# Performance work log

Hardware: AMD Instinct MI355X
Metric: run time of the kernel (lower is better)

Reference implementation:

```python
import jax, jax.numpy as jnp
import numpy as np

EPS = 1e-5  # BatchNorm eps
TOPK = 256  # SoftThresholdingOperation topk


def conv1x1(x, W, b):
    # x: [B,C,H,W], W: [O,C], b: [O]
    return jnp.einsum('bchw,oc->bohw', x, W) + b[None, :, None, None]


def bn_relu(x, gamma, beta, mean, var):
    # inference-mode BatchNorm2d followed by ReLU
    inv = gamma / jnp.sqrt(var + EPS)
    return jax.nn.relu(x * inv[None, :, None, None] + (beta - mean * inv)[None, :, None, None])


def topk_sparsemax(x, k):
    # HSPA SoftThresholdingOperation: sparsemax restricted to top-k entries of last axis.
    k = min(k, x.shape[-1])
    vals = jax.lax.top_k(x, k)[0]                       # sorted descending, [..., k]
    cssv = jnp.cumsum(vals, axis=-1) - 1.0              # cumulative sum minus 1
    r = jnp.arange(1, k + 1, dtype=x.dtype)
    support = vals * r > cssv                           # support indicator
    k_sup = jnp.sum(support, axis=-1, keepdims=True)    # support size, int
    tau = jnp.take_along_axis(cssv, k_sup - 1, axis=-1) / k_sup.astype(x.dtype)
    return jnp.clip(x - tau, 0.0)                       # sparse attention weights


def setup_inputs() -> dict:
    key = jax.random.key(0)
    ks = jax.random.split(key, 10)
    B, C = 128, 256
    s = 1.0 / np.sqrt(C)
    return {
        'zf': jax.random.normal(ks[0], (B, C, 13, 13), jnp.float32),
        'xf': jax.random.normal(ks[1], (B, C, 25, 25), jnp.float32),
        'Wq': jax.random.normal(ks[2], (C, C), jnp.float32) * s,
        'bq': jnp.zeros((C,), jnp.float32),
        'Ws': jax.random.normal(ks[3], (C, C), jnp.float32) * s,
        'bs': jnp.zeros((C,), jnp.float32),
        'Wg': jax.random.normal(ks[4], (C, C), jnp.float32) * s,
        'bg': jnp.zeros((C,), jnp.float32),
        'g_gamma': jnp.ones((C,), jnp.float32),
        'g_beta': jnp.zeros((C,), jnp.float32),
        'g_mean': jnp.zeros((C,), jnp.float32),
        'g_var': jnp.ones((C,), jnp.float32),
        'Wf': jax.random.normal(ks[5], (C, 2 * C), jnp.float32) * (1.0 / np.sqrt(2 * C)),
        'bf': jnp.zeros((C,), jnp.float32),
        'f_gamma': jnp.ones((C,), jnp.float32),
        'f_beta': jnp.zeros((C,), jnp.float32),
        'f_mean': jnp.zeros((C,), jnp.float32),
        'f_var': jnp.ones((C,), jnp.float32),
    }


def reference(zf, xf, Wq, bq, Ws, bs, Wg, bg, g_gamma, g_beta, g_mean, g_var,
              Wf, bf, f_gamma, f_beta, f_mean, f_var):
    B, C, Hx, Wx = xf.shape
    _, _, Hz, Wz = zf.shape
    xf_trans = conv1x1(xf, Wq, bq)                      # query
    zf_trans = conv1x1(zf, Ws, bs)                      # support
    xf_g = bn_relu(conv1x1(xf, Wg, bg), g_gamma, g_beta, g_mean, g_var)
    zf_g = bn_relu(conv1x1(zf, Wg, bg), g_gamma, g_beta, g_mean, g_var)

    Nx, Nz = Hx * Wx, Hz * Wz
    zf_trans_p = zf_trans.reshape(B, C, Nz)             # [B,C,Nz]
    zf_g_p = zf_g.reshape(B, C, Nz)                     # [B,C,Nz]
    xf_trans_p = xf_trans.reshape(B, C, Nx)             # [B,C,Nx]

    similar = jnp.einsum('bcn,bcm->bnm', xf_trans_p, zf_trans_p)  # [B,Nx,Nz]
    score = topk_sparsemax(similar, TOPK)                          # sparse attn
    embedding = jnp.einsum('bnm,bcm->bcn', score, zf_g_p)          # [B,C,Nx]
    embedding = embedding.reshape(B, C, Hx, Wx)

    cat = jnp.concatenate([embedding, xf_g], axis=1)    # [B,2C,Hx,Wx]
    out = bn_relu(conv1x1(cat, Wf, bf), f_gamma, f_beta, f_mean, f_var)
    return out
```

## Files before the change

kernel.cpp:

```cpp
#include <hip/hip_runtime.h>
#include <math.h>

#define EPS 1e-5f

constexpr int Bb  = 128;
constexpr int C   = 256;
constexpr int Nz  = 169;
constexpr int Nx  = 625;
constexpr int NzP = 192;

typedef __bf16 bf16x8 __attribute__((ext_vector_type(8)));
typedef float  f32x4  __attribute__((ext_vector_type(4)));

__device__ __forceinline__ unsigned short f2bf(float f) {
    union { float f; unsigned u; } x; x.f = f;
    unsigned r = x.u + 0x7FFFu + ((x.u >> 16) & 1u);
    return (unsigned short)(r >> 16);
}
__device__ __forceinline__ float bf2f(unsigned short h) {
    union { unsigned u; float f; } x; x.u = ((unsigned)h) << 16;
    return x.f;
}

__global__ __launch_bounds__(256)
void prep_all(const float* __restrict__ zf,
              const float* __restrict__ Wq, const float* __restrict__ bq,
              const float* __restrict__ Ws, const float* __restrict__ bs,
              const float* __restrict__ Wg, const float* __restrict__ Wf,
              unsigned short* __restrict__ Wg_bf, unsigned short* __restrict__ Wf_bf,
              float* __restrict__ wv, float* __restrict__ wu, float* __restrict__ c0,
              unsigned short* __restrict__ Mhi, unsigned short* __restrict__ Mlo,
              float* __restrict__ U,
              unsigned short* __restrict__ zfT_hi, unsigned short* __restrict__ zfT_lo)
{
    __shared__ float T[64][65];
    const int bx = blockIdx.x, tid = threadIdx.x;

    if (bx < 512) {
        int i = bx * 256 + tid;
        if (i < C * C) Wg_bf[i] = f2bf(Wg[i]);
        if (i < C * 2 * C) Wf_bf[i] = f2bf(Wf[i]);
        return;
    }
    if (bx == 512) {
        float a = 0.f, b = 0.f;
        for (int o = 0; o < C; ++o) {
            a += Wq[o * C + tid] * bs[o];
            b += Ws[o * C + tid] * bq[o];
        }
        wv[tid] = a;
        wu[tid] = b;
        if (tid == 0) {
            float c = 0.f;
            for (int o = 0; o < C; ++o) c += bq[o] * bs[o];
            c0[0] = c;
        }
        return;
    }
    if (bx < 529) {
        const int t  = bx - 513;
        const int j0 = (t & 3) * 64, i0 = (t >> 2) * 64;
        const int tx = tid & 15, ty = tid >> 4;
        float (*Qs)[65] = (float(*)[65])&T[0][0];
        float (*Ss)[65] = (float(*)[65])&T[16][0];
        float acc[4][4] = {};

        for (int kc = 0; kc < C; kc += 16) {
            #pragma unroll
            for (int i = 0; i < 4; ++i) {
                int e = tid + 256 * i;
                int k = e >> 6, col = e & 63;
                Qs[k][col] = Wq[(size_t)(kc + k) * C + i0 + col];
                Ss[k][col] = Ws[(size_t)(kc + k) * C + j0 + col];
            }
            __syncthreads();
            #pragma unroll
            for (int k = 0; k < 16; ++k) {
                float a[4], bv[4];
                #pragma unroll
                for (int i = 0; i < 4; ++i) a[i] = Qs[k][ty * 4 + i];
                #pragma unroll
                for (int j = 0; j < 4; ++j) bv[j] = Ss[k][tx * 4 + j];
                #pragma unroll
                for (int i = 0; i < 4; ++i)
                    #pragma unroll
                    for (int j = 0; j < 4; ++j)
                        acc[i][j] = fmaf(a[i], bv[j], acc[i][j]);
            }
            __syncthreads();
        }
        #pragma unroll
        for (int i = 0; i < 4; ++i)
            #pragma unroll
            for (int j = 0; j < 4; ++j) {
                float v = acc[i][j];
                unsigned short h = f2bf(v);
                size_t idx = (size_t)(i0 + ty * 4 + i) * C + j0 + tx * 4 + j;
                Mhi[idx] = h;
                Mlo[idx] = f2bf(v - bf2f(h));
            }
        return;
    }
    if (bx < 657) {
        const int b = bx - 529, m = tid;
        if (m >= NzP) return;
        float s = 0.f;
        if (m < Nz) {
            const float* zb = zf + (size_t)b * C * Nz + m;
            float s0 = 0.f, s1 = 0.f, s2 = 0.f, s3 = 0.f;
            for (int c = 0; c < C; c += 4) {
                s0 += wu[c]     * zb[(size_t)c * Nz];
                s1 += wu[c + 1] * zb[(size_t)(c + 1) * Nz];
                s2 += wu[c + 2] * zb[(size_t)(c + 2) * Nz];
                s3 += wu[c + 3] * zb[(size_t)(c + 3) * Nz];
            }
            s = (s0 + s1) + (s2 + s3) + c0[0];
        }
        U[(size_t)b * NzP + m] = s;
        return;
    }
    {
        const int t  = bx - 657;
        const int n0 = (t % 3) * 64;
        const int c0v = ((t / 3) & 3) * 64;
        const int b  = t / 12;
        const float* Xb = zf + ((size_t)b * C + c0v) * Nz;
        #pragma unroll
        for (int i = 0; i < 16; ++i) {
            int e = tid + 256 * i;
            int c = e >> 6, n = e & 63;
            T[c][n] = (n0 + n < Nz) ? Xb[(size_t)c * Nz + n0 + n] : 0.f;
        }
        __syncthreads();
        #pragma unroll
        for (int i = 0; i < 16; ++i) {
            int e = tid + 256 * i;
            int n = e >> 6, c = e & 63;
            if (n0 + n < Nz) {
                float v = T[c][n];
                unsigned short h = f2bf(v);
                size_t idx = ((size_t)b * Nz + n0 + n) * C + c0v + c;
                zfT_hi[idx] = h;
                zfT_lo[idx] = f2bf(v - bf2f(h));
            }
        }
    }
}

__global__ __launch_bounds__(256)
void z_gemm(const unsigned short* __restrict__ Mhi,
            const unsigned short* __restrict__ Mlo,
            const unsigned short* __restrict__ Wg,
            const unsigned short* __restrict__ Bhi,
            const unsigned short* __restrict__ Blo,
            const float* __restrict__ wv,
            const float* __restrict__ bg, const float* __restrict__ g_gamma,
            const float* __restrict__ g_beta, const float* __restrict__ g_mean,
            const float* __restrict__ g_var,
            unsigned short* __restrict__ Yqh, unsigned short* __restrict__ Yql,
            unsigned short* __restrict__ Yg)
{
    __shared__ unsigned short Ah[64][40], Al[64][40], Ag[64][40];
    __shared__ unsigned short Bh[64][40], Bl[64][40];

    const int b   = blockIdx.z;
    const int n0  = blockIdx.x * 64;
    const int o0  = blockIdx.y * 64;
    const int tid = threadIdx.x;
    const int lane = tid & 63, wid = tid >> 6;
    const int wr = wid >> 1, wc = wid & 1;

    const unsigned short* Bhb = Bhi + (size_t)b * Nz * C;
    const unsigned short* Blb = Blo + (size_t)b * Nz * C;

    f32x4 accq[2][2], accg[2][2];
    #pragma unroll
    for (int i = 0; i < 2; ++i)
        #pragma unroll
        for (int j = 0; j < 2; ++j)
            #pragma unroll
            for (int e = 0; e < 4; ++e) { accq[i][j][e] = 0.f; accg[i][j][e] = 0.f; }

    const int srow = tid >> 2, sseg = tid & 3;
    const int lr = lane & 15, lk = (lane >> 4) * 8;

    for (int kc = 0; kc < C; kc += 32) {
        const int gk = kc + sseg * 8;
        *(int4*)&Ah[srow][sseg * 8] = *(const int4*)&Mhi[(size_t)(o0 + srow) * C + gk];
        *(int4*)&Al[srow][sseg * 8] = *(const int4*)&Mlo[(size_t)(o0 + srow) * C + gk];
        *(int4*)&Ag[srow][sseg * 8] = *(const int4*)&Wg[(size_t)(o0 + srow) * C + gk];

        const int gn = n0 + srow;
        int4 bv = make_int4(0, 0, 0, 0), blv = make_int4(0, 0, 0, 0);
        if (gn < Nz) {
            bv  = *(const int4*)&Bhb[(size_t)gn * C + gk];
            blv = *(const int4*)&Blb[(size_t)gn * C + gk];
        }
        *(int4*)&Bh[srow][sseg * 8] = bv;
        *(int4*)&Bl[srow][sseg * 8] = blv;
        __syncthreads();

        bf16x8 ah[2], al[2], ag[2], bh[2], bl[2];
        #pragma unroll
        for (int i = 0; i < 2; ++i) {
            ah[i] = *(const bf16x8*)&Ah[wr * 32 + i * 16 + lr][lk];
            al[i] = *(const bf16x8*)&Al[wr * 32 + i * 16 + lr][lk];
            ag[i] = *(const bf16x8*)&Ag[wr * 32 + i * 16 + lr][lk];
            bh[i] = *(const bf16x8*)&Bh[wc * 32 + i * 16 + lr][lk];
            bl[i] = *(const bf16x8*)&Bl[wc * 32 + i * 16 + lr][lk];
        }
        #pragma unroll
        for (int i = 0; i < 2; ++i)
            #pragma unroll
            for (int j = 0; j < 2; ++j) {
                accq[i][j] = __builtin_amdgcn_mfma_f32_16x16x32_bf16(al[i], bh[j], accq[i][j], 0, 0, 0);
                accq[i][j] = __builtin_amdgcn_mfma_f32_16x16x32_bf16(ah[i], bl[j], accq[i][j], 0, 0, 0);
                accq[i][j] = __builtin_amdgcn_mfma_f32_16x16x32_bf16(ah[i], bh[j], accq[i][j], 0, 0, 0);
                accg[i][j] = __builtin_amdgcn_mfma_f32_16x16x32_bf16(ag[i], bh[j], accg[i][j], 0, 0, 0);
            }
        __syncthreads();
    }

    const int lg = lane >> 4;
    #pragma unroll
    for (int i = 0; i < 2; ++i) {
        const int ob = o0 + wr * 32 + i * 16 + lg * 4;
        float bi[4], inv[4], sh[4], bgi[4];
        #pragma unroll
        for (int r = 0; r < 4; ++r) {
            int o = ob + r;
            bi[r] = wv[o];
            float iv = g_gamma[o] * rsqrtf(g_var[o] + EPS);
            inv[r] = iv; sh[r] = g_beta[o] - g_mean[o] * iv; bgi[r] = bg[o];
        }
        #pragma unroll
        for (int j = 0; j < 2; ++j) {
            const int gn = n0 + wc * 32 + j * 16 + lr;
            uint2 ph = make_uint2(0, 0), pl = make_uint2(0, 0), pg = make_uint2(0, 0);
            if (gn < Nz) {
                unsigned short h[4], l[4], g[4];
                #pragma unroll
                for (int r = 0; r < 4; ++r) {
                    float v = accq[i][j][r] + bi[r];
                    h[r] = f2bf(v);
                    l[r] = f2bf(v - bf2f(h[r]));
                    g[r] = f2bf(fmaxf(fmaf(accg[i][j][r] + bgi[r], inv[r], sh[r]), 0.f));
                }
                ph.x = (unsigned)h[0] | ((unsigned)h[1] << 16);
                ph.y = (unsigned)h[2] | ((unsigned)h[3] << 16);
                pl.x = (unsigned)l[0] | ((unsigned)l[1] << 16);
                pl.y = (unsigned)l[2] | ((unsigned)l[3] << 16);
                pg.x = (unsigned)g[0] | ((unsigned)g[1] << 16);
                pg.y = (unsigned)g[2] | ((unsigned)g[3] << 16);
            }
            size_t idx = ((size_t)b * NzP + gn) * C + ob;
            *(uint2*)&Yqh[idx] = ph;
            *(uint2*)&Yql[idx] = pl;
            *(uint2*)&Yg[idx]  = pg;
        }
    }
}

__global__ __launch_bounds__(256)
void zg2_gemm(const unsigned short* __restrict__ A, int aLd,
              const unsigned short* __restrict__ B1,
              unsigned short* __restrict__ Y, int N, int Nout, int K, int O)
{
    __shared__ unsigned short As[64][40];
    __shared__ unsigned short Bs[64][40];

    const int b   = blockIdx.z;
    const int n0  = blockIdx.x * 64;
    const int o0  = blockIdx.y * 64;
    const int tid = threadIdx.x;
    const int lane = tid & 63, wid = tid >> 6;
    const int wr = wid >> 1, wc = wid & 1;

    const unsigned short* B1b = B1 + (size_t)b * N * K;

    f32x4 acc[2][2];
    #pragma unroll
    for (int i = 0; i < 2; ++i)
        #pragma unroll
        for (int j = 0; j < 2; ++j)
            #pragma unroll
            for (int e = 0; e < 4; ++e) acc[i][j][e] = 0.f;

    const int srow = tid >> 2, sseg = tid & 3;
    const int lr = lane & 15, lk = (lane >> 4) * 8;

    for (int kc = 0; kc < K; kc += 32) {
        const int gk = kc + sseg * 8;
        *(int4*)&As[srow][sseg * 8] = *(const int4*)&A[(size_t)(o0 + srow) * aLd + gk];

        const int gn = n0 + srow;
        int4 bv = make_int4(0, 0, 0, 0);
        if (gn < N) bv = *(const int4*)&B1b[(size_t)gn * K + gk];
        *(int4*)&Bs[srow][sseg * 8] = bv;
        __syncthreads();

        bf16x8 a0 = *(const bf16x8*)&As[wr * 32 +      lr][lk];
        bf16x8 a1 = *(const bf16x8*)&As[wr * 32 + 16 + lr][lk];
        bf16x8 b0 = *(const bf16x8*)&Bs[wc * 32 +      lr][lk];
        bf16x8 b1 = *(const bf16x8*)&Bs[wc * 32 + 16 + lr][lk];

        acc[0][0] = __builtin_amdgcn_mfma_f32_16x16x32_bf16(a0, b0, acc[0][0], 0, 0, 0);
        acc[0][1] = __builtin_amdgcn_mfma_f32_16x16x32_bf16(a0, b1, acc[0][1], 0, 0, 0);
        acc[1][0] = __builtin_amdgcn_mfma_f32_16x16x32_bf16(a1, b0, acc[1][0], 0, 0, 0);
        acc[1][1] = __builtin_amdgcn_mfma_f32_16x16x32_bf16(a1, b1, acc[1][1], 0, 0, 0);
        __syncthreads();
    }

    const int lg = lane >> 4;
    #pragma unroll
    for (int i = 0; i < 2; ++i) {
        const int ob = o0 + wr * 32 + i * 16 + lg * 4;
        #pragma unroll
        for (int j = 0; j < 2; ++j) {
            const int gn = n0 + wc * 32 + j * 16 + lr;
            if (gn < Nout) {
                #pragma unroll
                for (int r = 0; r < 4; ++r)
                    Y[((size_t)b * O + ob + r) * Nout + gn] =
                        (gn < N) ? f2bf(acc[i][j][r]) : (unsigned short)0;
            }
        }
    }
}

#define XGIDX(n, o) ((((n) << 8) + (o)) ^ (((n) & 7) << 3))

__global__ __launch_bounds__(256)
void mega_x(const float* __restrict__ Xf,
            const unsigned short* __restrict__ Zqh,
            const unsigned short* __restrict__ Zql,
            const unsigned short* __restrict__ Wg,
            const unsigned short* __restrict__ Zg2,
            const unsigned short* __restrict__ Wf2,
            const float* __restrict__ U,
            const float* __restrict__ bg, const float* __restrict__ g_gamma,
            const float* __restrict__ g_beta, const float* __restrict__ g_mean,
            const float* __restrict__ g_var,
            const float* __restrict__ bf, const float* __restrict__ f_gamma,
            const float* __restrict__ f_beta, const float* __restrict__ f_mean,
            const float* __restrict__ f_var,
            float* __restrict__ out)
{
    __shared__ __attribute__((aligned(16))) char pool[73728];
    __shared__ float Us[192];

    unsigned short* Bzh = (unsigned short*)(pool);
    unsigned short* Bzl = (unsigned short*)(pool + 15360);
    unsigned short* Ssc = (unsigned short*)(pool);
    unsigned short* XFh = (unsigned short*)(pool + 30720);
    unsigned short* XFl = (unsigned short*)(pool + 35840);
    unsigned short* XFg = (unsigned short*)(pool + 30720);
    unsigned short* XG  = (unsigned short*)(pool + 40960);

    const int g0  = blockIdx.z * gridDim.x + blockIdx.x;
    const int rid = (g0 & 7) * 160 + (g0 >> 3);
    const int b   = rid / 10;
    const int n0  = (rid % 10) * 64;

    const int tid = threadIdx.x;
    const int lane = tid & 63, w = tid >> 6;
    const int lr = lane & 15, lg = lane >> 4, lk = lg * 8;
    const int brow = tid >> 2, bseg = tid & 3;

    const unsigned short* Zqhb = Zqh + (size_t)b * NzP * C;
    const unsigned short* Zqlb = Zql + (size_t)b * NzP * C;
    const unsigned short* Zg2b = Zg2 + (size_t)b * C * NzP;

    if (tid < 192) Us[tid] = U[(size_t)b * NzP + tid];

    {
        f32x4 sacc[12];
        #pragma unroll
        for (int j = 0; j < 12; ++j)
            #pragma unroll
            for (int e = 0; e < 4; ++e) sacc[j][e] = 0.f;

        for (int kc = 0; kc < C; kc += 32) {
            {
                const int gn = min(n0 + brow, Nx - 1);
                const float* src = Xf + ((size_t)b * C + kc + bseg * 8) * Nx + gn;
                unsigned short h[8], l[8];
                #pragma unroll
                for (int e = 0; e < 8; ++e) {
                    float v = src[(size_t)e * Nx];
                    h[e] = f2bf(v);
                    l[e] = f2bf(v - bf2f(h[e]));
                }
                uint4 ph, pl;
                ph.x = (unsigned)h[0] | ((unsigned)h[1] << 16);
                ph.y = (unsigned)h[2] | ((unsigned)h[3] << 16);
                ph.z = (unsigned)h[4] | ((unsigned)h[5] << 16);
                ph.w = (unsigned)h[6] | ((unsigned)h[7] << 16);
                pl.x = (unsigned)l[0] | ((unsigned)l[1] << 16);
                pl.y = (unsigned)l[2] | ((unsigned)l[3] << 16);
                pl.z = (unsigned)l[4] | ((unsigned)l[5] << 16);
                pl.w = (unsigned)l[6] | ((unsigned)l[7] << 16);
                *(uint4*)&XFh[brow * 40 + bseg * 8] = ph;
                *(uint4*)&XFl[brow * 40 + bseg * 8] = pl;
            }
            #pragma unroll
            for (int i = 0; i < 3; ++i) {
                const int slot = tid + 256 * i;
                const int r = slot >> 2, s = slot & 3;
                const int gk = kc + s * 8;
                *(int4*)&Bzh[r * 40 + s * 8] = *(const int4*)&Zqhb[(size_t)r * C + gk];
                *(int4*)&Bzl[r * 40 + s * 8] = *(const int4*)&Zqlb[(size_t)r * C + gk];
            }
            __syncthreads();

            bf16x8 a0h = *(const bf16x8*)&XFh[(w * 16 + lr) * 40 + lk];
            bf16x8 a0l = *(const bf16x8*)&XFl[(w * 16 + lr) * 40 + lk];
            #pragma unroll
            for (int j = 0; j < 12; ++j) {
                bf16x8 bh = *(const bf16x8*)&Bzh[(j * 16 + lr) * 40 + lk];
                bf16x8 bl = *(const bf16x8*)&Bzl[(j * 16 + lr) * 40 + lk];
                sacc[j] = __builtin_amdgcn_mfma_f32_16x16x32_bf16(a0l, bh, sacc[j], 0, 0, 0);
                sacc[j] = __builtin_amdgcn_mfma_f32_16x16x32_bf16(a0h, bl, sacc[j], 0, 0, 0);
                sacc[j] = __builtin_amdgcn_mfma_f32_16x16x32_bf16(a0h, bh, sacc[j], 0, 0, 0);
            }
            __syncthreads();
        }

        #pragma unroll
        for (int j = 0; j < 12; ++j) {
            const int m = j * 16 + lr;
            const float uv = Us[m];
            const bool bad = (m >= Nz);
            #pragma unroll
            for (int q = 0; q < 4; ++q)
                sacc[j][q] = bad ? -1e30f : (sacc[j][q] + uv);
        }

        f32x4 mx = sacc[0];
        #pragma unroll
        for (int j = 1; j < 12; ++j)
            #pragma unroll
            for (int q = 0; q < 4; ++q) mx[q] = fmaxf(mx[q], sacc[j][q]);
        #pragma unroll
        for (int off = 1; off < 16; off <<= 1)
            #pragma unroll
            for (int q = 0; q < 4; ++q) mx[q] = fmaxf(mx[q], __shfl_xor(mx[q], off));

        f32x4 tau;
        #pragma unroll
        for (int q = 0; q < 4; ++q) tau[q] = mx[q] - 1.0f;

        for (int it = 0; it < 16; ++it) {
            f32x4 s, cnt;
            #pragma unroll
            for (int q = 0; q < 4; ++q) { s[q] = 0.f; cnt[q] = 0.f; }
            #pragma unroll
            for (int j = 0; j < 12; ++j)
                #pragma unroll
                for (int q = 0; q < 4; ++q)
                    if (sacc[j][q] > tau[q]) { s[q] += sacc[j][q]; cnt[q] += 1.f; }
            #pragma unroll
            for (int off = 1; off < 16; off <<= 1)
                #pragma unroll
                for (int q = 0; q < 4; ++q) {
                    s[q]   += __shfl_xor(s[q], off);
                    cnt[q] += __shfl_xor(cnt[q], off);
                }
            bool adv = false;
            #pragma unroll
            for (int q = 0; q < 4; ++q) {
                float nt = (s[q] - 1.0f) / cnt[q];
                if (nt > tau[q]) { tau[q] = nt; adv = true; }
            }
            if (!__any(adv ? 1 : 0)) break;
        }

        #pragma unroll
        for (int q = 0; q < 4; ++q) {
            const int n = w * 16 + 4 * lg + q;
            #pragma unroll
            for (int j = 0; j < 12; ++j) {
                const int m = j * 16 + lr;
                float sv = (m < Nz) ? fmaxf(sacc[j][q] - tau[q], 0.f) : 0.f;
                Ssc[n * 200 + m] = f2bf(sv);
            }
        }
    }

    f32x4 acc[4][4];
    #pragma unroll
    for (int i = 0; i < 4; ++i)
        #pragma unroll
        for (int j = 0; j < 4; ++j)
            #pragma unroll
            for (int e = 0; e < 4; ++e) acc[i][j][e] = 0.f;

    {
        const int gn = min(n0 + brow, Nx - 1);
        const float* src = Xf + ((size_t)b * C + bseg * 8) * Nx + gn;
        unsigned short h[8];
        #pragma unroll
        for (int e = 0; e < 8; ++e) h[e] = f2bf(src[(size_t)e * Nx]);
        uint4 ph;
        ph.x = (unsigned)h[0] | ((unsigned)h[1] << 16);
        ph.y = (unsigned)h[2] | ((unsigned)h[3] << 16);
        ph.z = (unsigned)h[4] | ((unsigned)h[5] << 16);
        ph.w = (unsigned)h[6] | ((unsigned)h[7] << 16);
        *(uint4*)&XFg[brow * 40 + bseg * 8] = ph;
    }
    __syncthreads();

    #pragma unroll
    for (int c = 0; c < 8; ++c) {
        const int kc = c * 32;
        if (c < 7) {
            const int gn = min(n0 + brow, Nx - 1);
            const float* src = Xf + ((size_t)b * C + kc + 32 + bseg * 8) * Nx + gn;
            unsigned short h[8];
            #pragma unroll
            for (int e = 0; e < 8; ++e) h[e] = f2bf(src[(size_t)e * Nx]);
            uint4 ph;
            ph.x = (unsigned)h[0] | ((unsigned)h[1] << 16);
            ph.y = (unsigned)h[2] | ((unsigned)h[3] << 16);
            ph.z = (unsigned)h[4] | ((unsigned)h[5] << 16);
            ph.w = (unsigned)h[6] | ((unsigned)h[7] << 16);
            *(uint4*)&XFg[((c + 1) & 1) * 2560 + brow * 40 + bseg * 8] = ph;
        }
        bf16x8 a[4], bfr[4];
        #pragma unroll
        for (int i = 0; i < 4; ++i)
            a[i] = *(const bf16x8*)&Wg[(size_t)(w * 64 + i * 16 + lr) * C + kc + lk];
        #pragma unroll
        for (int j = 0; j < 4; ++j)
            bfr[j] = *(const bf16x8*)&XFg[(c & 1) * 2560 + (j * 16 + lr) * 40 + lk];
        #pragma unroll
        for (int i = 0; i < 4; ++i)
            #pragma unroll
            for (int j = 0; j < 4; ++j)
                acc[i][j] = __builtin_amdgcn_mfma_f32_16x16x32_bf16(a[i], bfr[j], acc[i][j], 0, 0, 0);
        __syncthreads();
    }

    #pragma unroll
    for (int i = 0; i < 4; ++i) {
        const int ob = w * 64 + i * 16 + lg * 4;
        float inv[4], sh[4], bi[4];
        #pragma unroll
        for (int r = 0; r < 4; ++r) {
            int o = ob + r;
            float iv = g_gamma[o] * rsqrtf(g_var[o] + EPS);
            inv[r] = iv; sh[r] = g_beta[o] - g_mean[o] * iv; bi[r] = bg[o];
        }
        #pragma unroll
        for (int j = 0; j < 4; ++j) {
            const int n = j * 16 + lr;
            unsigned short h[4];
            #pragma unroll
            for (int r = 0; r < 4; ++r)
                h[r] = f2bf(fmaxf(fmaf(acc[i][j][r] + bi[r], inv[r], sh[r]), 0.f));
            uint2 pk;
            pk.x = (unsigned)h[0] | ((unsigned)h[1] << 16);
            pk.y = (unsigned)h[2] | ((unsigned)h[3] << 16);
            *(uint2*)&XG[XGIDX(n, ob)] = pk;
        }
    }
    #pragma unroll
    for (int i = 0; i < 4; ++i)
        #pragma unroll
        for (int j = 0; j < 4; ++j)
            #pragma unroll
            for (int e = 0; e < 4; ++e) acc[i][j][e] = 0.f;
    __syncthreads();

    #pragma unroll
    for (int c = 0; c < 6; ++c) {
        const int kc = c * 32;
        bf16x8 a[4], bfr[4];
        #pragma unroll
        for (int i = 0; i < 4; ++i)
            a[i] = *(const bf16x8*)&Zg2b[(size_t)(w * 64 + i * 16 + lr) * NzP + kc + lk];
        #pragma unroll
        for (int j = 0; j < 4; ++j)
            bfr[j] = *(const bf16x8*)&Ssc[(j * 16 + lr) * 200 + kc + lk];
        #pragma unroll
        for (int i = 0; i < 4; ++i)
            #pragma unroll
            for (int j = 0; j < 4; ++j)
                acc[i][j] = __builtin_amdgcn_mfma_f32_16x16x32_bf16(a[i], bfr[j], acc[i][j], 0, 0, 0);
    }

    #pragma unroll
    for (int c = 0; c < 8; ++c) {
        const int kc = c * 32;
        bf16x8 a[4], bfr[4];
        #pragma unroll
        for (int i = 0; i < 4; ++i)
            a[i] = *(const bf16x8*)&Wf2[(size_t)(w * 64 + i * 16 + lr) * 512 + kc + lk];
        #pragma unroll
        for (int j = 0; j < 4; ++j)
            bfr[j] = *(const bf16x8*)&XG[XGIDX(j * 16 + lr, kc + lk)];
        #pragma unroll
        for (int i = 0; i < 4; ++i)
            #pragma unroll
            for (int j = 0; j < 4; ++j)
                acc[i][j] = __builtin_amdgcn_mfma_f32_16x16x32_bf16(a[i], bfr[j], acc[i][j], 0, 0, 0);
    }

    #pragma unroll
    for (int i = 0; i < 4; ++i) {
        const int ob = w * 64 + i * 16 + lg * 4;
        float inv[4], sh[4], bi[4];
        #pragma unroll
        for (int r = 0; r < 4; ++r) {
            int o = ob + r;
            float iv = f_gamma[o] * rsqrtf(f_var[o] + EPS);
            inv[r] = iv; sh[r] = f_beta[o] - f_mean[o] * iv; bi[r] = bf[o];
        }
        #pragma unroll
        for (int j = 0; j < 4; ++j) {
            const int gn = n0 + j * 16 + lr;
            if (gn < Nx) {
                #pragma unroll
                for (int r = 0; r < 4; ++r) {
                    float v = fmaxf(fmaf(acc[i][j][r] + bi[r], inv[r], sh[r]), 0.f);
                    out[((size_t)b * C + ob + r) * Nx + gn] = v;
                }
            }
        }
    }
}

extern "C" void kernel_launch(void* const* d_in, const int* in_sizes, int n_in,
                              void* d_out, int out_size, void* d_ws, size_t ws_size,
                              hipStream_t stream)
{
    const float* zf      = (const float*)d_in[0];
    const float* xf      = (const float*)d_in[1];
    const float* Wq      = (const float*)d_in[2];
    const float* bq      = (const float*)d_in[3];
    const float* Ws_     = (const float*)d_in[4];
    const float* bs      = (const float*)d_in[5];
    const float* Wg      = (const float*)d_in[6];
    const float* bg      = (const float*)d_in[7];
    const float* g_gamma = (const float*)d_in[8];
    const float* g_beta  = (const float*)d_in[9];
    const float* g_mean  = (const float*)d_in[10];
    const float* g_var   = (const float*)d_in[11];
    const float* Wf      = (const float*)d_in[12];
    const float* bf_     = (const float*)d_in[13];
    const float* f_gamma = (const float*)d_in[14];
    const float* f_beta  = (const float*)d_in[15];
    const float* f_mean  = (const float*)d_in[16];
    const float* f_var   = (const float*)d_in[17];
    float* out = (float*)d_out;

    typedef unsigned short u16;
    char* ws = (char*)d_ws;
    u16*   zfT_hi = (u16*)(ws);
    u16*   zfT_lo = (u16*)(ws +  11075584);
    u16*   zqT_hi = (u16*)(ws +  22151168);
    u16*   zqT_lo = (u16*)(ws +  34734080);
    u16*   zf_gT  = (u16*)(ws +  47316992);
    u16*   zg2    = (u16*)(ws +  59899904);
    float* U      = (float*)(ws +  72482816);
    u16*   Mhi    = (u16*)(ws +  72581120);
    u16*   Mlo    = (u16*)(ws +  72712192);
    u16*   Wg_bf  = (u16*)(ws +  72843264);
    u16*   Wf_bf  = (u16*)(ws +  72974336);
    float* wv     = (float*)(ws +  73236480);
    float* wu     = (float*)(ws +  73237504);
    float* c0     = (float*)(ws +  73238528);

    dim3 blk(256);
    const int gx_x = (Nx + 63) / 64;
    const int gx_z = NzP / 64;

    prep_all<<<dim3(2193), blk, 0, stream>>>(
        zf, Wq, bq, Ws_, bs, Wg, Wf,
        Wg_bf, Wf_bf, wv, wu, c0, Mhi, Mlo, U, zfT_hi, zfT_lo);

    z_gemm<<<dim3(gx_z, C / 64, Bb), blk, 0, stream>>>(
        Mhi, Mlo, Wg_bf, zfT_hi, zfT_lo, wv,
        bg, g_gamma, g_beta, g_mean, g_var,
        zqT_hi, zqT_lo, zf_gT);

    zg2_gemm<<<dim3(gx_z, C / 64, Bb), blk, 0, stream>>>(
        Wf_bf, 2 * C, zf_gT, zg2, NzP, NzP, C, C);

    mega_x<<<dim3(gx_x, 1, Bb), blk, 0, stream>>>(
        xf, zqT_hi, zqT_lo, Wg_bf, zg2, Wf_bf + C, U,
        bg, g_gamma, g_beta, g_mean, g_var,
        bf_, f_gamma, f_beta, f_mean, f_var, out);
}
```

Before: 210.6 us.

## Keep full bf16 Xf tile in LDS and prefetch next chunk into registers

The bf16-high part of the 64x256 Xf tile is now kept resident in shared memory during the similarity GEMM, so the later Wg conv reuses it instead of reloading and reconverting Xf from global memory. The similarity loop is also software-pipelined: the next K-chunk of Xf and Zq is loaded into registers before the MFMAs run, then written to LDS afterwards, with the low part double-buffered. The Wg loop loses its per-iteration barriers. The cost is slightly more LDS and more registers live across the MFMA loop, which may reduce occupancy.

```diff
diff --git a/kernel.cpp b/kernel.cpp
--- a/kernel.cpp
+++ b/kernel.cpp
@@ -346,16 +346,15 @@
             const float* __restrict__ f_var,
             float* __restrict__ out)
 {
-    __shared__ __attribute__((aligned(16))) char pool[73728];
+    __shared__ __attribute__((aligned(16))) char pool[74752];
     __shared__ float Us[192];
 
-    unsigned short* Bzh = (unsigned short*)(pool);
-    unsigned short* Bzl = (unsigned short*)(pool + 15360);
-    unsigned short* Ssc = (unsigned short*)(pool);
-    unsigned short* XFh = (unsigned short*)(pool + 30720);
-    unsigned short* XFl = (unsigned short*)(pool + 35840);
-    unsigned short* XFg = (unsigned short*)(pool + 30720);
-    unsigned short* XG  = (unsigned short*)(pool + 40960);
+    unsigned short* XFfull = (unsigned short*)(pool);
+    unsigned short* XG     = (unsigned short*)(pool);
+    unsigned short* Bzh    = (unsigned short*)(pool + 33792);
+    unsigned short* Bzl    = (unsigned short*)(pool + 49152);
+    unsigned short* Ssc    = (unsigned short*)(pool + 33792);
+    unsigned short* XFl    = (unsigned short*)(pool + 64512);
 
     const int g0  = blockIdx.z * gridDim.x + blockIdx.x;
     const int rid = (g0 & 7) * 160 + (g0 >> 3);
@@ -373,6 +372,8 @@
 
     if (tid < 192) Us[tid] = U[(size_t)b * NzP + tid];
 
+    const int gnA = min(n0 + brow, Nx - 1);
+
     {
         f32x4 sacc[12];
         #pragma unroll
@@ -380,16 +381,72 @@
             #pragma unroll
             for (int e = 0; e < 4; ++e) sacc[j][e] = 0.f;
 
-        for (int kc = 0; kc < C; kc += 32) {
-            {
-                const int gn = min(n0 + brow, Nx - 1);
-                const float* src = Xf + ((size_t)b * C + kc + bseg * 8) * Nx + gn;
+        {
+            const float* src = Xf + ((size_t)b * C + bseg * 8) * Nx + gnA;
+            unsigned short h[8], l[8];
+            #pragma unroll
+            for (int e = 0; e < 8; ++e) {
+                float v = src[(size_t)e * Nx];
+                h[e] = f2bf(v);
+                l[e] = f2bf(v - bf2f(h[e]));
+            }
+            uint4 ph, pl;
+            ph.x = (unsigned)h[0] | ((unsigned)h[1] << 16);
+            ph.y = (unsigned)h[2] | ((unsigned)h[3] << 16);
+            ph.z = (unsigned)h[4] | ((unsigned)h[5] << 16);
+            ph.w = (unsigned)h[6] | ((unsigned)h[7] << 16);
+            pl.x = (unsigned)l[0] | ((unsigned)l[1] << 16);
+            pl.y = (unsigned)l[2] | ((unsigned)l[3] << 16);
+            pl.z = (unsigned)l[4] | ((unsigned)l[5] << 16);
+            pl.w = (unsigned)l[6] | ((unsigned)l[7] << 16);
+            *(uint4*)&XFfull[brow * 264 + bseg * 8] = ph;
+            *(uint4*)&XFl[brow * 40 + bseg * 8] = pl;
+            #pragma unroll
+            for (int i = 0; i < 3; ++i) {
+                const int slot = tid + 256 * i;
+                const int r = slot >> 2, s = slot & 3;
+                *(int4*)&Bzh[r * 40 + s * 8] = *(const int4*)&Zqhb[(size_t)r * C + s * 8];
+                *(int4*)&Bzl[r * 40 + s * 8] = *(const int4*)&Zqlb[(size_t)r * C + s * 8];
+            }
+        }
+        __syncthreads();
+
+        for (int c = 0; c < 8; ++c) {
+            const int kc = c * 32;
+            float xfr[8];
+            int4 pzh[3], pzl[3];
+            if (c < 7) {
+                const int kc1 = kc + 32;
+                const float* src = Xf + ((size_t)b * C + kc1 + bseg * 8) * Nx + gnA;
+                #pragma unroll
+                for (int e = 0; e < 8; ++e) xfr[e] = src[(size_t)e * Nx];
+                #pragma unroll
+                for (int i = 0; i < 3; ++i) {
+                    const int slot = tid + 256 * i;
+                    const int r = slot >> 2, s = slot & 3;
+                    pzh[i] = *(const int4*)&Zqhb[(size_t)r * C + kc1 + s * 8];
+                    pzl[i] = *(const int4*)&Zqlb[(size_t)r * C + kc1 + s * 8];
+                }
+            }
+
+            bf16x8 a0h = *(const bf16x8*)&XFfull[(w * 16 + lr) * 264 + kc + lk];
+            bf16x8 a0l = *(const bf16x8*)&XFl[(c & 1) * 2560 + (w * 16 + lr) * 40 + lk];
+            #pragma unroll
+            for (int j = 0; j < 12; ++j) {
+                bf16x8 bh = *(const bf16x8*)&Bzh[(j * 16 + lr) * 40 + lk];
+                bf16x8 bl = *(const bf16x8*)&Bzl[(j * 16 + lr) * 40 + lk];
+                sacc[j] = __builtin_amdgcn_mfma_f32_16x16x32_bf16(a0l, bh, sacc[j], 0, 0, 0);
+                sacc[j] = __builtin_amdgcn_mfma_f32_16x16x32_bf16(a0h, bl, sacc[j], 0, 0, 0);
+                sacc[j] = __builtin_amdgcn_mfma_f32_16x16x32_bf16(a0h, bh, sacc[j], 0, 0, 0);
+            }
+            __syncthreads();
+
+            if (c < 7) {
                 unsigned short h[8], l[8];
                 #pragma unroll
                 for (int e = 0; e < 8; ++e) {
-                    float v = src[(size_t)e * Nx];
-                    h[e] = f2bf(v);
-                    l[e] = f2bf(v - bf2f(h[e]));
+                    h[e] = f2bf(xfr[e]);
+                    l[e] = f2bf(xfr[e] - bf2f(h[e]));
                 }
                 uint4 ph, pl;
                 ph.x = (unsigned)h[0] | ((unsigned)h[1] << 16);
@@ -400,30 +457,17 @@
                 pl.y = (unsigned)l[2] | ((unsigned)l[3] << 16);
                 pl.z = (unsigned)l[4] | ((unsigned)l[5] << 16);
                 pl.w = (unsigned)l[6] | ((unsigned)l[7] << 16);
-                *(uint4*)&XFh[brow * 40 + bseg * 8] = ph;
-                *(uint4*)&XFl[brow * 40 + bseg * 8] = pl;
-            }
-            #pragma unroll
-            for (int i = 0; i < 3; ++i) {
-                const int slot = tid + 256 * i;
-                const int r = slot >> 2, s = slot & 3;
-                const int gk = kc + s * 8;
-                *(int4*)&Bzh[r * 40 + s * 8] = *(const int4*)&Zqhb[(size_t)r * C + gk];
-                *(int4*)&Bzl[r * 40 + s * 8] = *(const int4*)&Zqlb[(size_t)r * C + gk];
-            }
-            __syncthreads();
-
-            bf16x8 a0h = *(const bf16x8*)&XFh[(w * 16 + lr) * 40 + lk];
-            bf16x8 a0l = *(const bf16x8*)&XFl[(w * 16 + lr) * 40 + lk];
-            #pragma unroll
-            for (int j = 0; j < 12; ++j) {
-                bf16x8 bh = *(const bf16x8*)&Bzh[(j * 16 + lr) * 40 + lk];
-                bf16x8 bl = *(const bf16x8*)&Bzl[(j * 16 + lr) * 40 + lk];
-                sacc[j] = __builtin_amdgcn_mfma_f32_16x16x32_bf16(a0l, bh, sacc[j], 0, 0, 0);
-                sacc[j] = __builtin_amdgcn_mfma_f32_16x16x32_bf16(a0h, bl, sacc[j], 0, 0, 0);
-                sacc[j] = __builtin_amdgcn_mfma_f32_16x16x32_bf16(a0h, bh, sacc[j], 0, 0, 0);
-            }
-            __syncthreads();
+                *(uint4*)&XFfull[brow * 264 + (kc + 32) + bseg * 8] = ph;
+                *(uint4*)&XFl[((c + 1) & 1) * 2560 + brow * 40 + bseg * 8] = pl;
+                #pragma unroll
+                for (int i = 0; i < 3; ++i) {
+                    const int slot = tid + 256 * i;
+                    const int r = slot >> 2, s = slot & 3;
+                    *(int4*)&Bzh[r * 40 + s * 8] = pzh[i];
+                    *(int4*)&Bzl[r * 40 + s * 8] = pzl[i];
+                }
+                __syncthreads();
+            }
         }
 
         #pragma unroll
@@ -495,51 +539,23 @@
             #pragma unroll
             for (int e = 0; e < 4; ++e) acc[i][j][e] = 0.f;
 
-    {
-        const int gn = min(n0 + brow, Nx - 1);
-        const float* src = Xf + ((size_t)b * C + bseg * 8) * Nx + gn;
-        unsigned short h[8];
-        #pragma unroll
-        for (int e = 0; e < 8; ++e) h[e] = f2bf(src[(size_t)e * Nx]);
-        uint4 ph;
-        ph.x = (unsigned)h[0] | ((unsigned)h[1] << 16);
-        ph.y = (unsigned)h[2] | ((unsigned)h[3] << 16);
-        ph.z = (unsigned)h[4] | ((unsigned)h[5] << 16);
-        ph.w = (unsigned)h[6] | ((unsigned)h[7] << 16);
-        *(uint4*)&XFg[brow * 40 + bseg * 8] = ph;
-    }
-    __syncthreads();
-
     #pragma unroll
     for (int c = 0; c < 8; ++c) {
         const int kc = c * 32;
-        if (c < 7) {
-            const int gn = min(n0 + brow, Nx - 1);
-            const float* src = Xf + ((size_t)b * C + kc + 32 + bseg * 8) * Nx + gn;
-            unsigned short h[8];
-            #pragma unroll
-            for (int e = 0; e < 8; ++e) h[e] = f2bf(src[(size_t)e * Nx]);
-            uint4 ph;
-            ph.x = (unsigned)h[0] | ((unsigned)h[1] << 16);
-            ph.y = (unsigned)h[2] | ((unsigned)h[3] << 16);
-            ph.z = (unsigned)h[4] | ((unsigned)h[5] << 16);
-            ph.w = (unsigned)h[6] | ((unsigned)h[7] << 16);
-            *(uint4*)&XFg[((c + 1) & 1) * 2560 + brow * 40 + bseg * 8] = ph;
-        }
         bf16x8 a[4], bfr[4];
         #pragma unroll
         for (int i = 0; i < 4; ++i)
             a[i] = *(const bf16x8*)&Wg[(size_t)(w * 64 + i * 16 + lr) * C + kc + lk];
         #pragma unroll
         for (int j = 0; j < 4; ++j)
-            bfr[j] = *(const bf16x8*)&XFg[(c & 1) * 2560 + (j * 16 + lr) * 40 + lk];
+            bfr[j] = *(const bf16x8*)&XFfull[(j * 16 + lr) * 264 + kc + lk];
         #pragma unroll
         for (int i = 0; i < 4; ++i)
             #pragma unroll
             for (int j = 0; j < 4; ++j)
                 acc[i][j] = __builtin_amdgcn_mfma_f32_16x16x32_bf16(a[i], bfr[j], acc[i][j], 0, 0, 0);
-        __syncthreads();
-    }
+    }
+    __syncthreads();
 
     #pragma unroll
     for (int i = 0; i < 4; ++i) {
```

Result: slower. 225.7 us (+7.2%).

## Keep full bf16 Xf tile in LDS to reuse for the Wg conv

Applied to the files above, without the earlier changes.

The high bf16 half of the Xf tile, produced during the similarity GEMM, is now kept for all 256 channels in a padded LDS buffer instead of a per-chunk staging buffer. The later Wg projection reads this stored tile instead of reloading Xf from global memory, reconverting it and double-buffering it, so seven per-chunk barriers go away. The LDS pool is rearranged and shrinks slightly. XG aliases the full tile and is only written after the barrier that follows the conv loop.

```diff
diff --git a/kernel.cpp b/kernel.cpp
--- a/kernel.cpp
+++ b/kernel.cpp
@@ -346,16 +346,15 @@
             const float* __restrict__ f_var,
             float* __restrict__ out)
 {
-    __shared__ __attribute__((aligned(16))) char pool[73728];
+    __shared__ __attribute__((aligned(16))) char pool[69632];
     __shared__ float Us[192];
 
-    unsigned short* Bzh = (unsigned short*)(pool);
-    unsigned short* Bzl = (unsigned short*)(pool + 15360);
-    unsigned short* Ssc = (unsigned short*)(pool);
-    unsigned short* XFh = (unsigned short*)(pool + 30720);
-    unsigned short* XFl = (unsigned short*)(pool + 35840);
-    unsigned short* XFg = (unsigned short*)(pool + 30720);
-    unsigned short* XG  = (unsigned short*)(pool + 40960);
+    unsigned short* XFfull = (unsigned short*)(pool);
+    unsigned short* XG     = (unsigned short*)(pool);
+    unsigned short* Bzh    = (unsigned short*)(pool + 33792);
+    unsigned short* Bzl    = (unsigned short*)(pool + 49152);
+    unsigned short* Ssc    = (unsigned short*)(pool + 33792);
+    unsigned short* XFl    = (unsigned short*)(pool + 64512);
 
     const int g0  = blockIdx.z * gridDim.x + blockIdx.x;
     const int rid = (g0 & 7) * 160 + (g0 >> 3);
@@ -373,6 +372,8 @@
 
     if (tid < 192) Us[tid] = U[(size_t)b * NzP + tid];
 
+    const int gnA = min(n0 + brow, Nx - 1);
+
     {
         f32x4 sacc[12];
         #pragma unroll
@@ -382,8 +383,7 @@
 
         for (int kc = 0; kc < C; kc += 32) {
             {
-                const int gn = min(n0 + brow, Nx - 1);
-                const float* src = Xf + ((size_t)b * C + kc + bseg * 8) * Nx + gn;
+                const float* src = Xf + ((size_t)b * C + kc + bseg * 8) * Nx + gnA;
                 unsigned short h[8], l[8];
                 #pragma unroll
                 for (int e = 0; e < 8; ++e) {
@@ -400,7 +400,7 @@
                 pl.y = (unsigned)l[2] | ((unsigned)l[3] << 16);
                 pl.z = (unsigned)l[4] | ((unsigned)l[5] << 16);
                 pl.w = (unsigned)l[6] | ((unsigned)l[7] << 16);
-                *(uint4*)&XFh[brow * 40 + bseg * 8] = ph;
+                *(uint4*)&XFfull[brow * 264 + kc + bseg * 8] = ph;
                 *(uint4*)&XFl[brow * 40 + bseg * 8] = pl;
             }
             #pragma unroll
@@ -413,7 +413,7 @@
             }
             __syncthreads();
 
-            bf16x8 a0h = *(const bf16x8*)&XFh[(w * 16 + lr) * 40 + lk];
+            bf16x8 a0h = *(const bf16x8*)&XFfull[(w * 16 + lr) * 264 + kc + lk];
             bf16x8 a0l = *(const bf16x8*)&XFl[(w * 16 + lr) * 40 + lk];
             #pragma unroll
             for (int j = 0; j < 12; ++j) {
@@ -495,51 +495,23 @@
             #pragma unroll
             for (int e = 0; e < 4; ++e) acc[i][j][e] = 0.f;
 
-    {
-        const int gn = min(n0 + brow, Nx - 1);
-        const float* src = Xf + ((size_t)b * C + bseg * 8) * Nx + gn;
-        unsigned short h[8];
-        #pragma unroll
-        for (int e = 0; e < 8; ++e) h[e] = f2bf(src[(size_t)e * Nx]);
-        uint4 ph;
-        ph.x = (unsigned)h[0] | ((unsigned)h[1] << 16);
-        ph.y = (unsigned)h[2] | ((unsigned)h[3] << 16);
-        ph.z = (unsigned)h[4] | ((unsigned)h[5] << 16);
-        ph.w = (unsigned)h[6] | ((unsigned)h[7] << 16);
-        *(uint4*)&XFg[brow * 40 + bseg * 8] = ph;
-    }
-    __syncthreads();
-
     #pragma unroll
     for (int c = 0; c < 8; ++c) {
         const int kc = c * 32;
-        if (c < 7) {
-            const int gn = min(n0 + brow, Nx - 1);
-            const float* src = Xf + ((size_t)b * C + kc + 32 + bseg * 8) * Nx + gn;
-            unsigned short h[8];
-            #pragma unroll
-            for (int e = 0; e < 8; ++e) h[e] = f2bf(src[(size_t)e * Nx]);
-            uint4 ph;
-            ph.x = (unsigned)h[0] | ((unsigned)h[1] << 16);
-            ph.y = (unsigned)h[2] | ((unsigned)h[3] << 16);
-            ph.z = (unsigned)h[4] | ((unsigned)h[5] << 16);
-            ph.w = (unsigned)h[6] | ((unsigned)h[7] << 16);
-            *(uint4*)&XFg[((c + 1) & 1) * 2560 + brow * 40 + bseg * 8] = ph;
-        }
         bf16x8 a[4], bfr[4];
         #pragma unroll
         for (int i = 0; i < 4; ++i)
             a[i] = *(const bf16x8*)&Wg[(size_t)(w * 64 + i * 16 + lr) * C + kc + lk];
         #pragma unroll
         for (int j = 0; j < 4; ++j)
-            bfr[j] = *(const bf16x8*)&XFg[(c & 1) * 2560 + (j * 16 + lr) * 40 + lk];
+            bfr[j] = *(const bf16x8*)&XFfull[(j * 16 + lr) * 264 + kc + lk];
         #pragma unroll
         for (int i = 0; i < 4; ++i)
             #pragma unroll
             for (int j = 0; j < 4; ++j)
                 acc[i][j] = __builtin_amdgcn_mfma_f32_16x16x32_bf16(a[i], bfr[j], acc[i][j], 0, 0, 0);
-        __syncthreads();
-    }
+    }
+    __syncthreads();
 
     #pragma unroll
     for (int i = 0; i < 4; ++i) {
```

After: 199.0 us. 1.06x faster.
